# Optimization experiments

Measured on AMD Instinct MI355X. Metric: run time of the kernel, lower is better.

## Reference

```python
import math
import jax, jax.numpy as jnp
import numpy as np

N = 1024          # num_gaussians
W = 256           # image width
H = 256           # image height
C = 1             # grayscale -> 1 channel
BD = 2.0          # init bound
EPS2D = 0.3       # gsplat low-pass filter on 2D covariance


def setup_inputs() -> dict:
    key = jax.random.key(0)
    ks = jax.random.split(key, 8)
    # grid-initialized means (matches _init_gaussians for 2dgs)
    grid_size = int(math.ceil(math.sqrt(N)))
    lin = jnp.linspace(-BD, BD, grid_size)
    gx, gy = jnp.meshgrid(lin, lin, indexing='xy')
    grid_xy = jnp.stack([gx.ravel(), gy.ravel()], axis=1)[:N]
    noise = (jax.random.uniform(ks[0], (N, 2)) - 0.5) * (2 * BD / grid_size) * 0.5
    means = jnp.concatenate([grid_xy + noise, jnp.zeros((N, 1))], axis=1)      # [N,3]
    scales = jnp.concatenate([jax.random.uniform(ks[1], (N, 2)) * 0.5 + 0.1,
                              jnp.full((N, 1), 0.01)], axis=1)                  # [N,3]
    quats = jax.random.uniform(ks[2], (N,)) * (2.0 * math.pi)                   # [N] in-plane angle
    rgbs = jax.scipy.special.logit(jax.random.uniform(ks[3], (N, C)) * 0.3 + 0.1)
    opacities = jax.scipy.special.logit(jax.random.uniform(ks[4], (N,)) * 0.5 + 0.1)
    fov_x = math.pi / 2.0
    focal = 0.5 * W / math.tan(0.5 * fov_x)
    viewmat = jnp.array([[1.0, 0.0, 0.0, 0.0],
                         [0.0, 1.0, 0.0, 0.0],
                         [0.0, 0.0, 1.0, 8.0],
                         [0.0, 0.0, 0.0, 1.0]], dtype=jnp.float32)
    K = jnp.array([[focal, 0.0, W / 2.0],
                   [0.0, focal, H / 2.0],
                   [0.0, 0.0, 1.0]], dtype=jnp.float32)
    return {"means": means, "quats": quats, "scales": scales, "rgbs": rgbs,
            "opacities": opacities, "viewmat": viewmat, "K": K}


def _render(means, quats, scales, rgbs, opacities, viewmat, K):
    Rv, t = viewmat[:3, :3], viewmat[:3, 3]
    p_cam = means @ Rv.T + t                                # [N,3] camera-space
    x, y, z = p_cam[:, 0], p_cam[:, 1], p_cam[:, 2]
    fx, fy, cx, cy = K[0, 0], K[1, 1], K[0, 2], K[1, 2]
    inv_z = 1.0 / z
    u = fx * x * inv_z + cx                                 # [N] pixel means
    v = fy * y * inv_z + cy

    # 3D covariance: rotation about z-axis by angle theta (2DGS disk)
    ct, st = jnp.cos(quats), jnp.sin(quats)
    zr, on = jnp.zeros_like(ct), jnp.ones_like(ct)
    R3 = jnp.stack([jnp.stack([ct, -st, zr], -1),
                    jnp.stack([st,  ct, zr], -1),
                    jnp.stack([zr,  zr, on], -1)], -2)      # [N,3,3]
    M = R3 * scales[:, None, :]                             # R @ diag(s)
    cov3 = M @ jnp.swapaxes(M, -1, -2)                      # [N,3,3]
    cov_cam = jnp.einsum('ij,njk,lk->nil', Rv, cov3, Rv)    # [N,3,3]

    # perspective projection Jacobian -> 2D covariance
    j0 = jnp.stack([fx * inv_z, zr, -fx * x * inv_z * inv_z], -1)
    j1 = jnp.stack([zr, fy * inv_z, -fy * y * inv_z * inv_z], -1)
    J = jnp.stack([j0, j1], -2)                             # [N,2,3]
    cov2 = jnp.einsum('nij,njk,nlk->nil', J, cov_cam, J)    # [N,2,2]
    a = cov2[:, 0, 0] + EPS2D
    b = cov2[:, 0, 1]
    c = cov2[:, 1, 1] + EPS2D
    det = a * c - b * b
    conic_a, conic_b, conic_c = c / det, -b / det, a / det  # inverse covariance

    op = jax.nn.sigmoid(opacities)                          # torch.sigmoid(self.opacities)
    colors = jax.nn.sigmoid(rgbs)                           # torch.sigmoid(self.rgbs)

    # global front-to-back depth sort
    order = jnp.argsort(z)
    u, v = u[order], v[order]
    ca, cb, cc = conic_a[order], conic_b[order], conic_c[order]
    op, colors = op[order], colors[order]

    # pixel centers
    px = jnp.arange(W, dtype=jnp.float32) + 0.5
    py = jnp.arange(H, dtype=jnp.float32) + 0.5
    gx, gy = jnp.meshgrid(px, py)                           # [H,W]
    dx = gx.ravel()[:, None] - u[None, :]                   # [P,N]
    dy = gy.ravel()[:, None] - v[None, :]
    sigma = 0.5 * (ca * dx * dx + cc * dy * dy) + cb * dx * dy
    alpha = jnp.clip(op * jnp.exp(-jnp.maximum(sigma, 0.0)), 0.0, 0.999)

    # alpha compositing: T_i = prod_{j<i} (1 - alpha_j)
    logT = jnp.cumsum(jnp.log1p(-alpha), axis=1)
    P = H * W
    T = jnp.exp(jnp.concatenate([jnp.zeros((P, 1), alpha.dtype), logT[:, :-1]], axis=1))
    weights = alpha * T                                     # [P,N]
    img = weights @ colors                                  # [P,C]
    return img.reshape(H, W, C).transpose(2, 0, 1)[None]    # [1,C,H,W]


def reference(means, quats, scales, rgbs, opacities, viewmat, K):
    return _render(means, quats, scales, rgbs, opacities, viewmat, K)
```

## Files before the change

kernel.cpp:

```cpp
#include <hip/hip_runtime.h>

#define NG     1024
#define IMG_W  256
#define IMG_H  256
#define NWAVE  16
#define LOG2E  1.44269504088896340736f
#define INV2PI 0.15915494309189533577f
#define CULL_E (-16.0f)
#define PXC    128.0f

#define CAP0 512
#define CAP1 832
#define CAP2 832
#define CAP3 512
#define OFF0 0
#define OFF1 512
#define OFF2 1344
#define OFF3 2176
#define LTOT 2688

__global__ __launch_bounds__(1024, 1) void gs_fused(
    const float* __restrict__ means, const float* __restrict__ quats,
    const float* __restrict__ scales, const float* __restrict__ rgbs,
    const float* __restrict__ opacities, const float* __restrict__ viewmat,
    const float* __restrict__ Kmat, float* __restrict__ out)
{
    __shared__ float4 sL[LTOT];
    __shared__ float  pcb[2][NWAVE][64];
    __shared__ float  pTb[2][NWAVE][64];
    __shared__ int    sCnt[4][NWAVE];

    const int tid  = threadIdx.x;
    const int wave = tid >> 6;
    const int lane = tid & 63;
    const int b    = blockIdx.x;
    const int r0 = (b + 64)  & 255;
    const int r1 = b;
    const int r2 = (b + 128) & 255;
    const int r3 = (b + 192) & 255;

    float R00=viewmat[0], R01=viewmat[1], R02=viewmat[2],  t0=viewmat[3];
    float R10=viewmat[4], R11=viewmat[5], R12=viewmat[6],  t1=viewmat[7];
    float R20=viewmat[8], R21=viewmat[9], R22=viewmat[10], t2=viewmat[11];
    float fx=Kmat[0], cx=Kmat[2], fy=Kmat[4], cy=Kmat[5];
    float m0=means[3*tid+0], m1=means[3*tid+1], m2=means[3*tid+2];
    float xc = R00*m0 + R01*m1 + R02*m2 + t0;
    float yc = R10*m0 + R11*m1 + R12*m2 + t1;
    float zc = R20*m0 + R21*m1 + R22*m2 + t2;
    float iz = __builtin_amdgcn_rcpf(zc);
    float u  = fx*xc*iz + cx;
    float v  = fy*yc*iz + cy;
    float qr = quats[tid] * INV2PI;
    float ct = __builtin_amdgcn_cosf(qr);
    float st = __builtin_amdgcn_sinf(qr);
    float s0=scales[3*tid+0], s1=scales[3*tid+1], s2=scales[3*tid+2];
    float c00 = ct*ct*s0*s0 + st*st*s1*s1;
    float c01 = ct*st*(s0*s0 - s1*s1);
    float c11 = st*st*s0*s0 + ct*ct*s1*s1;
    float c22 = s2*s2;
    float T00 = R00*c00 + R01*c01;
    float T01 = R00*c01 + R01*c11;
    float T02 = R02*c22;
    float T10 = R10*c00 + R11*c01;
    float T11 = R10*c01 + R11*c11;
    float T12 = R12*c22;
    float T20 = R20*c00 + R21*c01;
    float T21 = R20*c01 + R21*c11;
    float T22 = R22*c22;
    float V00 = T00*R00 + T01*R01 + T02*R02;
    float V01 = T00*R10 + T01*R11 + T02*R12;
    float V02 = T00*R20 + T01*R21 + T02*R22;
    float V11 = T10*R10 + T11*R11 + T12*R12;
    float V12 = T10*R20 + T11*R21 + T12*R22;
    float V22 = T20*R20 + T21*R21 + T22*R22;
    float j00 = fx*iz, j02 = -fx*xc*iz*iz;
    float j11 = fy*iz, j12 = -fy*yc*iz*iz;
    float w00 = V00*j00 + V02*j02;
    float w02 = V02*j00 + V22*j02;
    float w10 = V01*j11 + V02*j12;
    float w11 = V11*j11 + V12*j12;
    float w12 = V12*j11 + V22*j12;
    float a  = j00*w00 + j02*w02 + 0.3f;
    float bb = j00*w10 + j02*w12;
    float c  = j11*w11 + j12*w12 + 0.3f;
    float idet = __builtin_amdgcn_rcpf(a*c - bb*bb);
    float tex  = __builtin_amdgcn_exp2f(-opacities[tid]*LOG2E);
    float l2op = -__builtin_amdgcn_logf(1.0f + tex);
    float cex  = __builtin_amdgcn_exp2f(-rgbs[tid]*LOG2E);
    float col  = __builtin_amdgcn_rcpf(1.0f + cex);
    float Ax = -0.5f*LOG2E*c*idet;
    float Bb =  LOG2E*bb*idet;
    float Cy = -0.5f*LOG2E*a*idet;
    float Hv = bb * __builtin_amdgcn_rcpf(c);
    float ut = u - PXC;

    float Bp0, Cp0, Bp1, Cp1, Bp2, Cp2, Bp3, Cp3;
    int   k0, k1, k2, k3;
#define FOLD(J, RJ, BPJ, CPJ, KEEPJ) do {                                   \
        float dy = ((float)(RJ) + 0.5f) - v;                                \
        float C1 = __builtin_fmaf(Cy, dy*dy, l2op);                         \
        float Bd = Bb * dy;                                                 \
        BPJ = __builtin_fmaf(-(Ax+Ax), ut, Bd);                             \
        float tq = __builtin_fmaf(Ax, ut, -Bd);                             \
        CPJ = __builtin_fmaf(tq, ut, C1);                                   \
        float pxv = __builtin_fmaf(Hv, dy, ut);                             \
        float lo = (float)((J)*64) + 0.5f - PXC;                            \
        float pq = __builtin_fminf(__builtin_fmaxf(pxv, lo), lo + 63.0f);   \
        float em = __builtin_fmaf(__builtin_fmaf(Ax, pq, BPJ), pq, CPJ);    \
        KEEPJ = (em > CULL_E) ? 1 : 0;                                      \
    } while (0)
    FOLD(0, r0, Bp0, Cp0, k0);
    FOLD(1, r1, Bp1, Cp1, k1);
    FOLD(2, r2, Bp2, Cp2, k2);
    FOLD(3, r3, Bp3, Cp3, k3);
#undef FOLD

    unsigned long long bal0 = __ballot(k0);
    unsigned long long bal1 = __ballot(k1);
    unsigned long long bal2 = __ballot(k2);
    unsigned long long bal3 = __ballot(k3);
    if (lane == 0) {
        sCnt[0][wave] = __popcll(bal0);
        sCnt[1][wave] = __popcll(bal1);
        sCnt[2][wave] = __popcll(bal2);
        sCnt[3][wave] = __popcll(bal3);
    }
    __syncthreads();
    int base0=0, base1=0, base2=0, base3=0;
    int M0=0, M1=0, M2=0, M3=0;
    #pragma unroll
    for (int w = 0; w < NWAVE; ++w) {
        int c0=sCnt[0][w], c1=sCnt[1][w], c2=sCnt[2][w], c3=sCnt[3][w];
        if (w < wave) { base0+=c0; base1+=c1; base2+=c2; base3+=c3; }
        M0+=c0; M1+=c1; M2+=c2; M3+=c3;
    }
    unsigned long long below = (1ULL << lane) - 1ULL;
    {
        int o0 = base0 + __popcll(bal0 & below);
        int o1 = base1 + __popcll(bal1 & below);
        int o2 = base2 + __popcll(bal2 & below);
        int o3 = base3 + __popcll(bal3 & below);
        if (k0 && o0 < CAP0) sL[OFF0 + o0] = make_float4(Ax, Bp0, Cp0, col);
        if (k1 && o1 < CAP1) sL[OFF1 + o1] = make_float4(Ax, Bp1, Cp1, col);
        if (k2 && o2 < CAP2) sL[OFF2 + o2] = make_float4(Ax, Bp2, Cp2, col);
        if (k3 && o3 < CAP3) sL[OFF3 + o3] = make_float4(Ax, Bp3, Cp3, col);
    }
    __syncthreads();

    int Ms0 = M0 < CAP0 ? M0 : CAP0;
    int Ms1 = M1 < CAP1 ? M1 : CAP1;
    int Ms2 = M2 < CAP2 ? M2 : CAP2;
    int Ms3 = M3 < CAP3 ? M3 : CAP3;

#define COMPOSITE(J, OFFJ, MSJ, BUF) do {                                   \
        int seg = (MSJ + NWAVE - 1) >> 4;                                   \
        int n0  = wave * seg;                                               \
        int n1  = n0 + seg; if (n1 > MSJ) n1 = MSJ;                         \
        float p  = (float)((J)*64 + lane) + 0.5f - PXC;                     \
        float Tc = 1.0f, cc = 0.0f;                                         \
        _Pragma("unroll 4")                                                 \
        for (int n = n0; n < n1; ++n) {                                     \
            float4 G = sL[OFFJ + n];                                        \
            float e  = __builtin_fmaf(__builtin_fmaf(G.x, p, G.y), p, G.z); \
            float al = __builtin_amdgcn_exp2f(e);                           \
            float w  = al * Tc;                                             \
            cc = __builtin_fmaf(w, G.w, cc);                                \
            Tc -= w;                                                        \
        }                                                                   \
        pcb[BUF][wave][lane] = cc;                                          \
        pTb[BUF][wave][lane] = Tc;                                          \
    } while (0)
#define MERGE(BUF, RJ, J) do {                                              \
        float ca = pcb[BUF][0][tid];                                        \
        float Ta = pTb[BUF][0][tid];                                        \
        _Pragma("unroll")                                                   \
        for (int w = 1; w < NWAVE; ++w) {                                   \
            ca = __builtin_fmaf(Ta, pcb[BUF][w][tid], ca);                  \
            Ta *= pTb[BUF][w][tid];                                         \
        }                                                                   \
        out[(RJ) * IMG_W + (J)*64 + tid] = ca;                              \
    } while (0)

    COMPOSITE(0, OFF0, Ms0, 0);
    __syncthreads();
    COMPOSITE(1, OFF1, Ms1, 1);
    if (tid < 64) MERGE(0, r0, 0);
    __syncthreads();
    COMPOSITE(2, OFF2, Ms2, 0);
    if (tid < 64) MERGE(1, r1, 1);
    __syncthreads();
    COMPOSITE(3, OFF3, Ms3, 1);
    if (tid < 64) MERGE(0, r2, 2);
    __syncthreads();
    if (tid < 64) MERGE(1, r3, 3);
#undef COMPOSITE
#undef MERGE
}

extern "C" void kernel_launch(void* const* d_in, const int* in_sizes, int n_in,
                              void* d_out, int out_size, void* d_ws, size_t ws_size,
                              hipStream_t stream) {
    const float* means     = (const float*)d_in[0];
    const float* quats     = (const float*)d_in[1];
    const float* scales    = (const float*)d_in[2];
    const float* rgbs      = (const float*)d_in[3];
    const float* opacities = (const float*)d_in[4];
    const float* viewmat   = (const float*)d_in[5];
    const float* Kmat      = (const float*)d_in[6];
    float* out = (float*)d_out;

    gs_fused<<<IMG_H, 1024, 0, stream>>>(means, quats, scales, rgbs,
                                         opacities, viewmat, Kmat, out);
}
```

Before: 12.36 us.

## Factor covariance projection, add transmittance early exit, move merges to late waves

New measurement: 13.55 us. 9.7% more time.

```diff
diff --git a/kernel.cpp b/kernel.cpp
--- a/kernel.cpp
+++ b/kernel.cpp
@@ -50,39 +50,27 @@
     float iz = __builtin_amdgcn_rcpf(zc);
     float u  = fx*xc*iz + cx;
     float v  = fy*yc*iz + cy;
+    float j00 = fx*iz, j02 = -fx*xc*iz*iz;
+    float j11 = fy*iz, j12 = -fy*yc*iz*iz;
+    float P00 = j00*R00 + j02*R20;
+    float P01 = j00*R01 + j02*R21;
+    float P02 = j00*R02 + j02*R22;
+    float P10 = j11*R10 + j12*R20;
+    float P11 = j11*R11 + j12*R21;
+    float P12 = j11*R12 + j12*R22;
     float qr = quats[tid] * INV2PI;
     float ct = __builtin_amdgcn_cosf(qr);
     float st = __builtin_amdgcn_sinf(qr);
     float s0=scales[3*tid+0], s1=scales[3*tid+1], s2=scales[3*tid+2];
-    float c00 = ct*ct*s0*s0 + st*st*s1*s1;
-    float c01 = ct*st*(s0*s0 - s1*s1);
-    float c11 = st*st*s0*s0 + ct*ct*s1*s1;
-    float c22 = s2*s2;
-    float T00 = R00*c00 + R01*c01;
-    float T01 = R00*c01 + R01*c11;
-    float T02 = R02*c22;
-    float T10 = R10*c00 + R11*c01;
-    float T11 = R10*c01 + R11*c11;
-    float T12 = R12*c22;
-    float T20 = R20*c00 + R21*c01;
-    float T21 = R20*c01 + R21*c11;
-    float T22 = R22*c22;
-    float V00 = T00*R00 + T01*R01 + T02*R02;
-    float V01 = T00*R10 + T01*R11 + T02*R12;
-    float V02 = T00*R20 + T01*R21 + T02*R22;
-    float V11 = T10*R10 + T11*R11 + T12*R12;
-    float V12 = T10*R20 + T11*R21 + T12*R22;
-    float V22 = T20*R20 + T21*R21 + T22*R22;
-    float j00 = fx*iz, j02 = -fx*xc*iz*iz;
-    float j11 = fy*iz, j12 = -fy*yc*iz*iz;
-    float w00 = V00*j00 + V02*j02;
-    float w02 = V02*j00 + V22*j02;
-    float w10 = V01*j11 + V02*j12;
-    float w11 = V11*j11 + V12*j12;
-    float w12 = V12*j11 + V22*j12;
-    float a  = j00*w00 + j02*w02 + 0.3f;
-    float bb = j00*w10 + j02*w12;
-    float c  = j11*w11 + j12*w12 + 0.3f;
+    float Q00 = (P00*ct + P01*st) * s0;
+    float Q01 = (P01*ct - P00*st) * s1;
+    float Q02 = P02 * s2;
+    float Q10 = (P10*ct + P11*st) * s0;
+    float Q11 = (P11*ct - P10*st) * s1;
+    float Q12 = P12 * s2;
+    float a  = Q00*Q00 + Q01*Q01 + Q02*Q02 + 0.3f;
+    float bb = Q00*Q10 + Q01*Q11 + Q02*Q12;
+    float c  = Q10*Q10 + Q11*Q11 + Q12*Q12 + 0.3f;
     float idet = __builtin_amdgcn_rcpf(a*c - bb*bb);
     float tex  = __builtin_amdgcn_exp2f(-opacities[tid]*LOG2E);
     float l2op = -__builtin_amdgcn_logf(1.0f + tex);
@@ -158,41 +146,45 @@
         int n1  = n0 + seg; if (n1 > MSJ) n1 = MSJ;                         \
         float p  = (float)((J)*64 + lane) + 0.5f - PXC;                     \
         float Tc = 1.0f, cc = 0.0f;                                         \
-        _Pragma("unroll 4")                                                 \
-        for (int n = n0; n < n1; ++n) {                                     \
-            float4 G = sL[OFFJ + n];                                        \
-            float e  = __builtin_fmaf(__builtin_fmaf(G.x, p, G.y), p, G.z); \
-            float al = __builtin_amdgcn_exp2f(e);                           \
-            float w  = al * Tc;                                             \
-            cc = __builtin_fmaf(w, G.w, cc);                                \
-            Tc -= w;                                                        \
+        for (int ch = n0; ch < n1; ch += 8) {                               \
+            int ce = ch + 8; if (ce > n1) ce = n1;                          \
+            _Pragma("unroll 8")                                             \
+            for (int n = ch; n < ce; ++n) {                                 \
+                float4 G = sL[OFFJ + n];                                    \
+                float e  = __builtin_fmaf(__builtin_fmaf(G.x, p, G.y), p, G.z); \
+                float al = __builtin_amdgcn_exp2f(e);                       \
+                float w  = al * Tc;                                         \
+                cc = __builtin_fmaf(w, G.w, cc);                            \
+                Tc -= w;                                                    \
+            }                                                               \
+            if (__all(Tc < 1e-6f)) break;                                   \
         }                                                                   \
         pcb[BUF][wave][lane] = cc;                                          \
         pTb[BUF][wave][lane] = Tc;                                          \
     } while (0)
 #define MERGE(BUF, RJ, J) do {                                              \
-        float ca = pcb[BUF][0][tid];                                        \
-        float Ta = pTb[BUF][0][tid];                                        \
+        float ca = pcb[BUF][0][lane];                                       \
+        float Ta = pTb[BUF][0][lane];                                       \
         _Pragma("unroll")                                                   \
         for (int w = 1; w < NWAVE; ++w) {                                   \
-            ca = __builtin_fmaf(Ta, pcb[BUF][w][tid], ca);                  \
-            Ta *= pTb[BUF][w][tid];                                         \
+            ca = __builtin_fmaf(Ta, pcb[BUF][w][lane], ca);                 \
+            Ta *= pTb[BUF][w][lane];                                        \
         }                                                                   \
-        out[(RJ) * IMG_W + (J)*64 + tid] = ca;                              \
+        out[(RJ) * IMG_W + (J)*64 + lane] = ca;                             \
     } while (0)
 
     COMPOSITE(0, OFF0, Ms0, 0);
     __syncthreads();
     COMPOSITE(1, OFF1, Ms1, 1);
-    if (tid < 64) MERGE(0, r0, 0);
+    if (wave == 15) MERGE(0, r0, 0);
     __syncthreads();
     COMPOSITE(2, OFF2, Ms2, 0);
-    if (tid < 64) MERGE(1, r1, 1);
+    if (wave == 14) MERGE(1, r1, 1);
     __syncthreads();
     COMPOSITE(3, OFF3, Ms3, 1);
-    if (tid < 64) MERGE(0, r2, 2);
-    __syncthreads();
-    if (tid < 64) MERGE(1, r3, 3);
+    if (wave == 13) MERGE(0, r2, 2);
+    __syncthreads();
+    if (wave == 12) MERGE(1, r3, 3);
 #undef COMPOSITE
 #undef MERGE
 }
```
